# Performance work log

Measured on AMD Instinct MI355X. Metric: run time of the kernel, lower is better.

The kernel has to match this reference:

```python
import jax, jax.numpy as jnp
import numpy as np

N, E = 10000, 320000
IN, HID, HEADS, OUT = 128, 32, 8, 64
NEG_SLOPE = 0.2  # PyG GATv2Conv default negative_slope


def _glorot(k, shape):
    fan = shape[0] + shape[-1]
    return jax.random.normal(k, shape, jnp.float32) * (2.0 / fan) ** 0.5


def setup_inputs() -> dict:
    key = jax.random.key(0)
    ks = jax.random.split(key, 12)
    D2 = HEADS * HID  # 256
    inp = {
        "x": jax.random.normal(ks[0], (N, IN), jnp.float32),
        "edge_index": jax.random.randint(ks[1], (2, E), 0, N, jnp.int32),
        # layer 1: IN -> HID per head, HEADS heads, concat
        "Wl1": _glorot(ks[2], (IN, D2)), "bl1": jnp.zeros((D2,), jnp.float32),
        "Wr1": _glorot(ks[3], (IN, D2)), "br1": jnp.zeros((D2,), jnp.float32),
        "att1": _glorot(ks[4], (HEADS, HID)), "bias1": jnp.zeros((D2,), jnp.float32),
        # layer 2: D2 -> HID per head, HEADS heads, concat
        "Wl2": _glorot(ks[5], (D2, D2)), "bl2": jnp.zeros((D2,), jnp.float32),
        "Wr2": _glorot(ks[6], (D2, D2)), "br2": jnp.zeros((D2,), jnp.float32),
        "att2": _glorot(ks[7], (HEADS, HID)), "bias2": jnp.zeros((D2,), jnp.float32),
        # layer 3: D2 -> OUT, 1 head
        "Wl3": _glorot(ks[8], (D2, OUT)), "bl3": jnp.zeros((OUT,), jnp.float32),
        "Wr3": _glorot(ks[9], (D2, OUT)), "br3": jnp.zeros((OUT,), jnp.float32),
        "att3": _glorot(ks[10], (1, OUT)), "bias3": jnp.zeros((OUT,), jnp.float32),
    }
    return inp


def _segment_softmax(scores, seg, n):
    # softmax over edges grouped by destination node
    m = jax.ops.segment_max(scores, seg, num_segments=n)
    m = jnp.where(jnp.isfinite(m), m, 0.0)  # guard isolated nodes
    ex = jnp.exp(scores - m[seg])
    denom = jax.ops.segment_sum(ex, seg, num_segments=n)
    return ex / (denom[seg] + 1e-16)


def _gatv2_conv(x, src, dst, Wl, bl, Wr, br, att, bias, heads, ch, n):
    gl = (x @ Wl + bl).reshape(n, heads, ch)  # source-side transform [N,H,C]
    gr = (x @ Wr + br).reshape(n, heads, ch)  # target-side transform [N,H,C]
    e = jax.nn.leaky_relu(gl[src] + gr[dst], NEG_SLOPE)  # [E,H,C]
    score = jnp.einsum('ehc,hc->eh', e, att)  # per-edge per-head attention logits
    alpha = _segment_softmax(score, dst, n)  # [E,H]; attention dropout p=0.6 is identity in eval
    out = jax.ops.segment_sum(alpha[:, :, None] * gl[src], dst, num_segments=n)  # [N,H,C]
    return out.reshape(n, heads * ch) + bias


def reference(x, edge_index, Wl1, bl1, Wr1, br1, att1, bias1,
              Wl2, bl2, Wr2, br2, att2, bias2,
              Wl3, bl3, Wr3, br3, att3, bias3):
    src, dst = edge_index[0], edge_index[1]
    n = x.shape[0]
    # F.dropout(p=0.6) layers are identity in eval mode
    h = jax.nn.elu(_gatv2_conv(x, src, dst, Wl1, bl1, Wr1, br1, att1, bias1, HEADS, HID, n))
    h = jax.nn.elu(_gatv2_conv(h, src, dst, Wl2, bl2, Wr2, br2, att2, bias2, HEADS, HID, n))
    h = _gatv2_conv(h, src, dst, Wl3, bl3, Wr3, br3, att3, bias3, 1, OUT, n)
    return jax.nn.sigmoid(h)
```

## Files before the change

### kernel.cpp

```cpp
#include <hip/hip_runtime.h>
#include <math.h>

#define N_NODES 10000
#define N_EDGES 320000
#define D_IN    128
#define D2      256
#define HEADS   8
#define HID     32
#define D_OUT   64

typedef _Float16 h2 __attribute__((ext_vector_type(2)));

__device__ __forceinline__ float fdot2(h2 a, h2 b, float c) {
#if __has_builtin(__builtin_amdgcn_fdot2)
    return __builtin_amdgcn_fdot2(a, b, c, false);
#else
    return fmaf((float)a.x, (float)b.x, fmaf((float)a.y, (float)b.y, c));
#endif
}
__device__ __forceinline__ h2 bch2(unsigned u) { return __builtin_bit_cast(h2, u); }
__device__ __forceinline__ unsigned bcu(h2 v)  { return __builtin_bit_cast(unsigned, v); }
__device__ __forceinline__ unsigned packf(float a, float b) {
    h2 h = {(_Float16)a, (_Float16)b};
    return bcu(h);
}

__global__ void zero_deg(int* __restrict__ deg) {
    const int i = blockIdx.x * 256 + threadIdx.x;
    if (i < N_NODES) deg[i] = 0;
}

__global__ void prep_all(const float* __restrict__ x, unsigned* __restrict__ xh,
                         const float* __restrict__ a1, unsigned* __restrict__ a1h,
                         const float* __restrict__ a2, unsigned* __restrict__ a2h,
                         const float* __restrict__ W1l, const float* __restrict__ W1r,
                         const float* __restrict__ W2l, const float* __restrict__ W2r,
                         const float* __restrict__ W3l, const float* __restrict__ W3r,
                         unsigned* __restrict__ P1l, unsigned* __restrict__ P1r,
                         unsigned* __restrict__ P2l, unsigned* __restrict__ P2r,
                         unsigned* __restrict__ P3l, unsigned* __restrict__ P3r,
                         const int* __restrict__ ei, int* __restrict__ deg) {
    const int b = blockIdx.x, t = threadIdx.x;
    if (b < 2500) {
        const int i = b * 256 + t;
        const float2 f = *reinterpret_cast<const float2*>(&x[2 * i]);
        xh[i] = packf(f.x, f.y);
    } else if (b == 2500) {
        if (t < 128) a1h[t] = packf(a1[2 * t], a1[2 * t + 1]);
    } else if (b == 2501) {
        if (t < 128) a2h[t] = packf(a2[2 * t], a2[2 * t + 1]);
    } else if (b < 2950) {
        const int wb = b - 2502;
        const float* src; unsigned* dst; int M, idx;
        if (wb < 128)      { M = 256; const bool r = wb >= 64;  src = r ? W1r : W1l; dst = r ? P1r : P1l; idx = (wb & 63) * 256 + t; }
        else if (wb < 384) { M = 256; const bool r = wb >= 256; src = r ? W2r : W2l; dst = r ? P2r : P2l; idx = ((wb - 128) & 127) * 256 + t; }
        else               { M = 64;  const bool r = wb >= 416; src = r ? W3r : W3l; dst = r ? P3r : P3l; idx = ((wb - 384) & 31) * 256 + t; }
        const int kp = idx / M, c = idx - kp * M;
        dst[idx] = packf(src[(2 * kp) * M + c], src[(2 * kp + 1) * M + c]);
    } else {
        const int e = (b - 2950) * 256 + t;
        if (e < N_EDGES) atomicAdd(&deg[ei[N_EDGES + e]], 1);
    }
}

template<int K, bool HOUT>
__global__ __launch_bounds__(512) void gemm_dual_fd(
        const unsigned* __restrict__ Ah,
        const unsigned* __restrict__ Wpl, const float* __restrict__ bl,
        const unsigned* __restrict__ Wpr, const float* __restrict__ br,
        void* __restrict__ glv, void* __restrict__ grv,
        int Mtot, int nrows) {
    constexpr int BM = 64, BN = 64, KP = 16;
    constexpr int KPtot = K / 2;
    __shared__ unsigned As2[KP][BM + 1];
    __shared__ unsigned Wls[KP][BN + 4];
    __shared__ unsigned Wrs[KP][BN + 4];

    const int t  = threadIdx.x;
    const int tx = t & 15;
    const int ty = t >> 4;
    const int row0 = blockIdx.x * BM;
    const int col0 = blockIdx.y * BN;

    const int an  = t >> 3;
    const int aq2 = (t & 7) * 2;
    const int sel = t >> 8;
    const int wk  = (t >> 4) & 15;
    const int wc  = (t & 15) * 4;
    const unsigned* Wsrc = sel ? Wpr : Wpl;
    unsigned* wd = sel ? &Wrs[0][0] : &Wls[0][0];

    float aL[2][4], aR[2][4];
    {
        const float4 b4l = *reinterpret_cast<const float4*>(&bl[col0 + tx * 4]);
        const float4 b4r = *reinterpret_cast<const float4*>(&br[col0 + tx * 4]);
        const float bll[4] = {b4l.x, b4l.y, b4l.z, b4l.w};
        const float brr[4] = {b4r.x, b4r.y, b4r.z, b4r.w};
#pragma unroll
        for (int i = 0; i < 2; ++i)
#pragma unroll
            for (int j = 0; j < 4; ++j) { aL[i][j] = bll[j]; aR[i][j] = brr[j]; }
    }

    for (int k0p = 0; k0p < KPtot; k0p += KP) {
        __syncthreads();
        {
            const int row = row0 + an;
            uint2 v = make_uint2(0u, 0u);
            if (row < nrows) v = *reinterpret_cast<const uint2*>(&Ah[(size_t)row * KPtot + k0p + aq2]);
            As2[aq2 + 0][an] = v.x;
            As2[aq2 + 1][an] = v.y;
        }
        {
            const uint4 w = *reinterpret_cast<const uint4*>(&Wsrc[(size_t)(k0p + wk) * Mtot + col0 + wc]);
            *reinterpret_cast<uint4*>(&wd[wk * (BN + 4) + wc]) = w;
        }
        __syncthreads();

#pragma unroll
        for (int kp = 0; kp < KP; ++kp) {
            const h2 a0 = bch2(As2[kp][ty * 2 + 0]);
            const h2 a1 = bch2(As2[kp][ty * 2 + 1]);
            const uint4 lu = *reinterpret_cast<const uint4*>(&Wls[kp][tx * 4]);
            const uint4 ru = *reinterpret_cast<const uint4*>(&Wrs[kp][tx * 4]);
            const h2 l[4] = {bch2(lu.x), bch2(lu.y), bch2(lu.z), bch2(lu.w)};
            const h2 r[4] = {bch2(ru.x), bch2(ru.y), bch2(ru.z), bch2(ru.w)};
#pragma unroll
            for (int j = 0; j < 4; ++j) {
                aL[0][j] = fdot2(a0, l[j], aL[0][j]);
                aL[1][j] = fdot2(a1, l[j], aL[1][j]);
                aR[0][j] = fdot2(a0, r[j], aR[0][j]);
                aR[1][j] = fdot2(a1, r[j], aR[1][j]);
            }
        }
    }

#pragma unroll
    for (int i = 0; i < 2; ++i) {
        const int row = row0 + ty * 2 + i;
        if (row < nrows) {
            if constexpr (HOUT) {
                unsigned* glu = (unsigned*)glv;
                unsigned* gru = (unsigned*)grv;
                const size_t off = (size_t)row * (Mtot / 2) + (col0 + tx * 4) / 2;
                *reinterpret_cast<uint2*>(&glu[off]) =
                    make_uint2(packf(aL[i][0], aL[i][1]), packf(aL[i][2], aL[i][3]));
                *reinterpret_cast<uint2*>(&gru[off]) =
                    make_uint2(packf(aR[i][0], aR[i][1]), packf(aR[i][2], aR[i][3]));
            } else {
                float* glf = (float*)glv;
                float* grf = (float*)grv;
                const size_t off = (size_t)row * Mtot + col0 + tx * 4;
                *reinterpret_cast<float4*>(&glf[off]) = make_float4(aL[i][0], aL[i][1], aL[i][2], aL[i][3]);
                *reinterpret_cast<float4*>(&grf[off]) = make_float4(aR[i][0], aR[i][1], aR[i][2], aR[i][3]);
            }
        }
    }
}

__global__ void scan_rowptr(const int* __restrict__ deg,
                            int* __restrict__ row_ptr, int* __restrict__ cursor) {
    __shared__ int part[1024];
    const int t = threadIdx.x;
    const int base = t * 10;
    int loc[10];
    int s = 0;
#pragma unroll
    for (int i = 0; i < 10; ++i) {
        const int v = (base + i < N_NODES) ? deg[base + i] : 0;
        loc[i] = s; s += v;
    }
    part[t] = s;
    __syncthreads();
    for (int d = 1; d < 1024; d <<= 1) {
        const int v = (t >= d) ? part[t - d] : 0;
        __syncthreads();
        part[t] += v;
        __syncthreads();
    }
    const int off = (t > 0) ? part[t - 1] : 0;
#pragma unroll
    for (int i = 0; i < 10; ++i) {
        const int idx = base + i;
        if (idx < N_NODES) {
            const int r = off + loc[i];
            row_ptr[idx] = r; cursor[idx] = r;
        }
    }
    if (t == 0) row_ptr[N_NODES] = N_EDGES;
}

__global__ void scatter_edges(const int* __restrict__ ei, int* __restrict__ cursor,
                              int* __restrict__ esrc) {
    const int e = blockIdx.x * blockDim.x + threadIdx.x;
    if (e < N_EDGES) {
        const int pos = atomicAdd(&cursor[ei[N_EDGES + e]], 1);
        esrc[pos] = ei[e];
    }
}

__global__ __launch_bounds__(256) void gat_wave_h2(
        const int* __restrict__ row_ptr, const int* __restrict__ esrc,
        const unsigned* __restrict__ gl, const unsigned* __restrict__ gr,
        const unsigned* __restrict__ atth, const float* __restrict__ bias,
        unsigned* __restrict__ hout) {
    constexpr int MU = D2 / 2;
    const int wid  = threadIdx.x >> 6;
    const int lane = threadIdx.x & 63;
    const int half = lane >> 5;
    const int sub  = lane & 31;
    const int n = blockIdx.x * 4 + wid;
    if (n >= N_NODES) return;
    const int u4 = sub * 4;
    const int c0 = sub * 8;

    h2 grn[4], av[4];
    {
        const uint4 u = *reinterpret_cast<const uint4*>(&gr[(size_t)n * MU + u4]);
        grn[0] = bch2(u.x); grn[1] = bch2(u.y); grn[2] = bch2(u.z); grn[3] = bch2(u.w);
        const uint4 a = *reinterpret_cast<const uint4*>(&atth[u4]);
        av[0] = bch2(a.x); av[1] = bch2(a.y); av[2] = bch2(a.z); av[3] = bch2(a.w);
    }
    const h2 hz = {(_Float16)0.f, (_Float16)0.f};
    const h2 hp = {(_Float16)0.2f, (_Float16)0.2f};

    float acc[8] = {0.f, 0.f, 0.f, 0.f, 0.f, 0.f, 0.f, 0.f};
    float denom = 0.0f;

    const int beg = row_ptr[n], end = row_ptr[n + 1];

    for (int base = beg; base < end; base += 64) {
        const int len = min(64, end - base);
        const int npairs = (len + 1) >> 1;
        const int myid = (base + lane < end) ? esrc[base + lane] : 0;

        uint4 cur, nx1;
        {
            const int s0 = __shfl(myid, half);
            cur = *reinterpret_cast<const uint4*>(&gl[(size_t)s0 * MU + u4]);
        }
        if (npairs > 1) {
            const int s1 = __shfl(myid, 2 + half);
            nx1 = *reinterpret_cast<const uint4*>(&gl[(size_t)s1 * MU + u4]);
        } else nx1 = cur;

        for (int i = 0; i < npairs; ++i) {
            uint4 nx2 = cur;
            if (i + 2 < npairs) {
                const int s2 = __shfl(myid, 2 * (i + 2) + half);
                nx2 = *reinterpret_cast<const uint4*>(&gl[(size_t)s2 * MU + u4]);
            }

            const h2 G[4] = {bch2(cur.x), bch2(cur.y), bch2(cur.z), bch2(cur.w)};
            float s = 0.0f;
#pragma unroll
            for (int q = 0; q < 4; ++q) {
                const h2 v = G[q] + grn[q];
                const h2 lr = __builtin_elementwise_min(v, hz) * hp +
                              __builtin_elementwise_max(v, hz);
                s = fdot2(lr, av[q], s);
            }
            s += __shfl_xor(s, 1, 64);
            s += __shfl_xor(s, 2, 64);
            s = ((2 * i + half) < len) ? s : -INFINITY;

            const float e1 = __expf(s);
            denom += e1;
#pragma unroll
            for (int q = 0; q < 4; ++q) {
                acc[2*q]   = fmaf(e1, (float)G[q].x, acc[2*q]);
                acc[2*q+1] = fmaf(e1, (float)G[q].y, acc[2*q+1]);
            }
            cur = nx1; nx1 = nx2;
        }
    }

    denom += __shfl_xor(denom, 32, 64);
#pragma unroll
    for (int v2 = 0; v2 < 8; ++v2) acc[v2] += __shfl_xor(acc[v2], 32, 64);

    if (half == 0) {
        const float inv = 1.0f / (denom + 1e-16f);
        const float4 b0 = *reinterpret_cast<const float4*>(&bias[c0]);
        const float4 b1 = *reinterpret_cast<const float4*>(&bias[c0 + 4]);
        const float bb[8] = {b0.x, b0.y, b0.z, b0.w, b1.x, b1.y, b1.z, b1.w};
        float r[8];
#pragma unroll
        for (int v2 = 0; v2 < 8; ++v2) {
            float val = acc[v2] * inv + bb[v2];
            r[v2] = val > 0.0f ? val : expm1f(val);
        }
        uint4 o;
        o.x = packf(r[0], r[1]); o.y = packf(r[2], r[3]);
        o.z = packf(r[4], r[5]); o.w = packf(r[6], r[7]);
        *reinterpret_cast<uint4*>(&hout[(size_t)n * MU + u4]) = o;
    }
}

__global__ __launch_bounds__(256) void gat_group3(
        const int* __restrict__ row_ptr, const int* __restrict__ esrc,
        const float* __restrict__ gl, const float* __restrict__ gr,
        const float* __restrict__ att, const float* __restrict__ bias,
        float* __restrict__ out) {
    constexpr int M = 64;
    const int wid  = threadIdx.x >> 6;
    const int lane = threadIdx.x & 63;
    const int g    = lane >> 4;
    const int sub  = lane & 15;
    const int n = blockIdx.x * 16 + wid * 4 + g;
    const bool nvalid = (n < N_NODES);
    const int c0 = sub * 4;

    float grn[4], attc[4], acc[4] = {0.f, 0.f, 0.f, 0.f};
    {
        const size_t noff = (size_t)(nvalid ? n : 0) * M + c0;
        const float4 g4 = *reinterpret_cast<const float4*>(&gr[noff]);
        grn[0]=g4.x; grn[1]=g4.y; grn[2]=g4.z; grn[3]=g4.w;
        const float4 a4 = *reinterpret_cast<const float4*>(&att[c0]);
        attc[0]=a4.x; attc[1]=a4.y; attc[2]=a4.z; attc[3]=a4.w;
    }
    float denom = 0.0f;

    const int beg = nvalid ? row_ptr[n] : 0;
    const int deg = nvalid ? (row_ptr[n + 1] - beg) : 0;

    for (int off = 0; __any(off < deg); off += 16) {
        const int myid = (off + sub < deg) ? esrc[beg + off + sub] : 0;

        float4 cur;
        {
            const int src = __shfl(myid, (g << 4));
            cur = *reinterpret_cast<const float4*>(&gl[(size_t)src * M + c0]);
        }
#pragma unroll
        for (int j = 0; j < 16; ++j) {
            float4 nxt = make_float4(0.f, 0.f, 0.f, 0.f);
            if (j + 1 < 16) {
                const int ns = __shfl(myid, (g << 4) + j + 1);
                nxt = *reinterpret_cast<const float4*>(&gl[(size_t)ns * M + c0]);
            }
            const float gg[4] = {cur.x, cur.y, cur.z, cur.w};
            float s = 0.0f;
#pragma unroll
            for (int v = 0; v < 4; ++v) {
                const float val = gg[v] + grn[v];
                const float lr  = fmaxf(val, 0.0f) + 0.2f * fminf(val, 0.0f);
                s = fmaf(lr, attc[v], s);
            }
#pragma unroll
            for (int d = 1; d < 16; d <<= 1) s += __shfl_xor(s, d, 64);
            s = ((off + j) < deg) ? s : -INFINITY;

            const float e1 = __expf(s);
            denom += e1;
#pragma unroll
            for (int v = 0; v < 4; ++v) acc[v] = fmaf(e1, gg[v], acc[v]);
            cur = nxt;
        }
    }

    if (nvalid) {
        const float inv = 1.0f / (denom + 1e-16f);
        float4 r;
        r.x = 1.0f / (1.0f + __expf(-(acc[0] * inv + bias[c0 + 0])));
        r.y = 1.0f / (1.0f + __expf(-(acc[1] * inv + bias[c0 + 1])));
        r.z = 1.0f / (1.0f + __expf(-(acc[2] * inv + bias[c0 + 2])));
        r.w = 1.0f / (1.0f + __expf(-(acc[3] * inv + bias[c0 + 3])));
        *reinterpret_cast<float4*>(&out[(size_t)n * M + c0]) = r;
    }
}

extern "C" void kernel_launch(void* const* d_in, const int* in_sizes, int n_in,
                              void* d_out, int out_size, void* d_ws, size_t ws_size,
                              hipStream_t stream) {
    const float* x    = (const float*)d_in[0];
    const int*   ei   = (const int*)  d_in[1];
    const float* Wl1  = (const float*)d_in[2];
    const float* bl1  = (const float*)d_in[3];
    const float* Wr1  = (const float*)d_in[4];
    const float* br1  = (const float*)d_in[5];
    const float* att1 = (const float*)d_in[6];
    const float* bi1  = (const float*)d_in[7];
    const float* Wl2  = (const float*)d_in[8];
    const float* bl2  = (const float*)d_in[9];
    const float* Wr2  = (const float*)d_in[10];
    const float* br2  = (const float*)d_in[11];
    const float* att2 = (const float*)d_in[12];
    const float* bi2  = (const float*)d_in[13];
    const float* Wl3  = (const float*)d_in[14];
    const float* bl3  = (const float*)d_in[15];
    const float* Wr3  = (const float*)d_in[16];
    const float* br3  = (const float*)d_in[17];
    const float* att3 = (const float*)d_in[18];
    const float* bi3  = (const float*)d_in[19];

    float* out = (float*)d_out;

    unsigned* ws   = (unsigned*)d_ws;
    unsigned* xh   = ws;
    unsigned* gl16 = xh   + (size_t)N_NODES * 64;
    unsigned* gr16 = gl16 + (size_t)N_NODES * 128;
    unsigned* h16  = gr16 + (size_t)N_NODES * 128;
    float*    glf  = (float*)(h16 + (size_t)N_NODES * 128);
    float*    grf  = glf + (size_t)N_NODES * 64;
    unsigned* Wp1l = (unsigned*)(grf + (size_t)N_NODES * 64);
    unsigned* Wp1r = Wp1l + 16384;
    unsigned* Wp2l = Wp1r + 16384;
    unsigned* Wp2r = Wp2l + 32768;
    unsigned* Wp3l = Wp2r + 32768;
    unsigned* Wp3r = Wp3l + 8192;
    unsigned* ath1 = Wp3r + 8192;
    unsigned* ath2 = ath1 + 128;
    int* deg     = (int*)(ath2 + 128);
    int* row_ptr = deg + N_NODES;
    int* cursor  = row_ptr + N_NODES + 1;
    int* esrc    = cursor + N_NODES;

    zero_deg<<<(N_NODES + 255) / 256, 256, 0, stream>>>(deg);
    prep_all<<<2950 + (N_EDGES + 255) / 256, 256, 0, stream>>>(
        x, xh, att1, ath1, att2, ath2,
        Wl1, Wr1, Wl2, Wr2, Wl3, Wr3,
        Wp1l, Wp1r, Wp2l, Wp2r, Wp3l, Wp3r,
        ei, deg);
    scan_rowptr<<<1, 1024, 0, stream>>>(deg, row_ptr, cursor);
    scatter_edges<<<(N_EDGES + 255) / 256, 256, 0, stream>>>(ei, cursor, esrc);

    const int RT64 = (N_NODES + 63) / 64;

    gemm_dual_fd<D_IN, true><<<dim3(RT64, 4), 512, 0, stream>>>(
        xh, Wp1l, bl1, Wp1r, br1, gl16, gr16, D2, N_NODES);
    gat_wave_h2<<<(N_NODES + 3) / 4, 256, 0, stream>>>(
        row_ptr, esrc, gl16, gr16, ath1, bi1, h16);

    gemm_dual_fd<D2, true><<<dim3(RT64, 4), 512, 0, stream>>>(
        h16, Wp2l, bl2, Wp2r, br2, gl16, gr16, D2, N_NODES);
    gat_wave_h2<<<(N_NODES + 3) / 4, 256, 0, stream>>>(
        row_ptr, esrc, gl16, gr16, ath2, bi2, h16);

    gemm_dual_fd<D2, false><<<dim3(RT64, 1), 512, 0, stream>>>(
        h16, Wp3l, bl3, Wp3r, br3, glf, grf, D_OUT, N_NODES);
    gat_group3<<<(N_NODES + 15) / 16, 256, 0, stream>>>(
        row_ptr, esrc, glf, grf, att3, bi3, out);
}
```

Before: 203.3 us.

## Switch dual GEMMs to MFMA with transposed fp16 weights, deepen gather prefetch

Replaces the fdot2-based dual GEMM with a 16x16x32 f16 MFMA kernel. The prep stage now transposes the weights into fp16 column-major tiles through shared memory so they match the MFMA B-operand layout, and the whole A row-tile is staged in LDS once. The edge-gather loops in the layer-1/2 and layer-3 attention kernels also gain a deeper 4-deep register prefetch of source features. This trades scalar dot-product ALU work for matrix cores, at the cost of narrower scalar output stores and more live registers in the gather loops.

```diff
diff --git a/kernel.cpp b/kernel.cpp
--- a/kernel.cpp
+++ b/kernel.cpp
@@ -9,7 +9,9 @@
 #define HID     32
 #define D_OUT   64
 
-typedef _Float16 h2 __attribute__((ext_vector_type(2)));
+typedef _Float16 h2   __attribute__((ext_vector_type(2)));
+typedef _Float16 f16x8 __attribute__((ext_vector_type(8)));
+typedef float    f32x4 __attribute__((ext_vector_type(4)));
 
 __device__ __forceinline__ float fdot2(h2 a, h2 b, float c) {
 #if __has_builtin(__builtin_amdgcn_fdot2)
@@ -19,10 +21,9 @@
 #endif
 }
 __device__ __forceinline__ h2 bch2(unsigned u) { return __builtin_bit_cast(h2, u); }
-__device__ __forceinline__ unsigned bcu(h2 v)  { return __builtin_bit_cast(unsigned, v); }
 __device__ __forceinline__ unsigned packf(float a, float b) {
     h2 h = {(_Float16)a, (_Float16)b};
-    return bcu(h);
+    return __builtin_bit_cast(unsigned, h);
 }
 
 __global__ void zero_deg(int* __restrict__ deg) {
@@ -36,9 +37,9 @@
                          const float* __restrict__ W1l, const float* __restrict__ W1r,
                          const float* __restrict__ W2l, const float* __restrict__ W2r,
                          const float* __restrict__ W3l, const float* __restrict__ W3r,
-                         unsigned* __restrict__ P1l, unsigned* __restrict__ P1r,
-                         unsigned* __restrict__ P2l, unsigned* __restrict__ P2r,
-                         unsigned* __restrict__ P3l, unsigned* __restrict__ P3r,
+                         _Float16* __restrict__ T1l, _Float16* __restrict__ T1r,
+                         _Float16* __restrict__ T2l, _Float16* __restrict__ T2r,
+                         _Float16* __restrict__ T3l, _Float16* __restrict__ T3r,
                          const int* __restrict__ ei, int* __restrict__ deg) {
     const int b = blockIdx.x, t = threadIdx.x;
     if (b < 2500) {
@@ -49,110 +50,100 @@
         if (t < 128) a1h[t] = packf(a1[2 * t], a1[2 * t + 1]);
     } else if (b == 2501) {
         if (t < 128) a2h[t] = packf(a2[2 * t], a2[2 * t + 1]);
-    } else if (b < 2950) {
+    } else if (b < 2558) {
+        __shared__ float tl[64][65];
         const int wb = b - 2502;
-        const float* src; unsigned* dst; int M, idx;
-        if (wb < 128)      { M = 256; const bool r = wb >= 64;  src = r ? W1r : W1l; dst = r ? P1r : P1l; idx = (wb & 63) * 256 + t; }
-        else if (wb < 384) { M = 256; const bool r = wb >= 256; src = r ? W2r : W2l; dst = r ? P2r : P2l; idx = ((wb - 128) & 127) * 256 + t; }
-        else               { M = 64;  const bool r = wb >= 416; src = r ? W3r : W3l; dst = r ? P3r : P3l; idx = ((wb - 384) & 31) * 256 + t; }
-        const int kp = idx / M, c = idx - kp * M;
-        dst[idx] = packf(src[(2 * kp) * M + c], src[(2 * kp + 1) * M + c]);
+        const float* Wsrc; _Float16* Wdst; int K, M, tile;
+        if (wb < 16)      { K = 128; M = 256; const bool r = wb >= 8;  Wsrc = r ? W1r : W1l; Wdst = r ? T1r : T1l; tile = wb & 7; }
+        else if (wb < 48) { K = 256; M = 256; const bool r = wb >= 32; Wsrc = r ? W2r : W2l; Wdst = r ? T2r : T2l; tile = (wb - 16) & 15; }
+        else              { K = 256; M = 64;  const bool r = wb >= 52; Wsrc = r ? W3r : W3l; Wdst = r ? T3r : T3l; tile = (wb - 48) & 3; }
+        const int ktiles = K >> 6;
+        const int k0 = (tile % ktiles) * 64, c0 = (tile / ktiles) * 64;
+        const int rr = t >> 6, cc = t & 63;
+        for (int i = 0; i < 64; i += 4)
+            tl[i + rr][cc] = Wsrc[(size_t)(k0 + i + rr) * M + c0 + cc];
+        __syncthreads();
+        for (int i = 0; i < 64; i += 4)
+            Wdst[(size_t)(c0 + i + rr) * K + k0 + cc] = (_Float16)tl[cc][i + rr];
     } else {
-        const int e = (b - 2950) * 256 + t;
+        const int e = (b - 2558) * 256 + t;
         if (e < N_EDGES) atomicAdd(&deg[ei[N_EDGES + e]], 1);
     }
 }
 
 template<int K, bool HOUT>
-__global__ __launch_bounds__(512) void gemm_dual_fd(
+__global__ __launch_bounds__(256) void gemm_dual_mfma(
         const unsigned* __restrict__ Ah,
-        const unsigned* __restrict__ Wpl, const float* __restrict__ bl,
-        const unsigned* __restrict__ Wpr, const float* __restrict__ br,
+        const _Float16* __restrict__ Wtl, const float* __restrict__ bl,
+        const _Float16* __restrict__ Wtr, const float* __restrict__ br,
         void* __restrict__ glv, void* __restrict__ grv,
         int Mtot, int nrows) {
-    constexpr int BM = 64, BN = 64, KP = 16;
-    constexpr int KPtot = K / 2;
-    __shared__ unsigned As2[KP][BM + 1];
-    __shared__ unsigned Wls[KP][BN + 4];
-    __shared__ unsigned Wrs[KP][BN + 4];
-
-    const int t  = threadIdx.x;
-    const int tx = t & 15;
-    const int ty = t >> 4;
-    const int row0 = blockIdx.x * BM;
-    const int col0 = blockIdx.y * BN;
-
-    const int an  = t >> 3;
-    const int aq2 = (t & 7) * 2;
-    const int sel = t >> 8;
-    const int wk  = (t >> 4) & 15;
-    const int wc  = (t & 15) * 4;
-    const unsigned* Wsrc = sel ? Wpr : Wpl;
-    unsigned* wd = sel ? &Wrs[0][0] : &Wls[0][0];
-
-    float aL[2][4], aR[2][4];
+    constexpr int AS = K + 8;
+    __shared__ __align__(16) _Float16 Asm[64 * AS];
+    __shared__ __align__(16) _Float16 Wsm[2][64 * 40];
+
+    const int t = threadIdx.x;
+    const int wave = t >> 6, lane = t & 63;
+    const int lrow = lane & 15, lgrp = lane >> 4;
+    const int row0 = blockIdx.x * 64, col0 = blockIdx.y * 64;
+
     {
-        const float4 b4l = *reinterpret_cast<const float4*>(&bl[col0 + tx * 4]);
-        const float4 b4r = *reinterpret_cast<const float4*>(&br[col0 + tx * 4]);
-        const float bll[4] = {b4l.x, b4l.y, b4l.z, b4l.w};
-        const float brr[4] = {b4r.x, b4r.y, b4r.z, b4r.w};
-#pragma unroll
-        for (int i = 0; i < 2; ++i)
-#pragma unroll
-            for (int j = 0; j < 4; ++j) { aL[i][j] = bll[j]; aR[i][j] = brr[j]; }
-    }
-
-    for (int k0p = 0; k0p < KPtot; k0p += KP) {
+        constexpr int CPR = K / 8;
+        const int ar = t / CPR, ac = t % CPR;
+        for (int i = 0; i < 64; i += 256 / CPR) {
+            const int row = row0 + i + ar;
+            uint4 v = make_uint4(0u, 0u, 0u, 0u);
+            if (row < nrows) v = *reinterpret_cast<const uint4*>(&Ah[(size_t)row * (K / 2) + ac * 4]);
+            *reinterpret_cast<uint4*>(&Asm[(i + ar) * AS + ac * 8]) = v;
+        }
+    }
+
+    f32x4 accL[4], accR[4];
+#pragma unroll
+    for (int cf = 0; cf < 4; ++cf) { accL[cf] = (f32x4)0.0f; accR[cf] = (f32x4)0.0f; }
+
+    const int wcol = t >> 2, wch = t & 3;
+
+    for (int ks = 0; ks < K / 32; ++ks) {
         __syncthreads();
         {
-            const int row = row0 + an;
-            uint2 v = make_uint2(0u, 0u);
-            if (row < nrows) v = *reinterpret_cast<const uint2*>(&Ah[(size_t)row * KPtot + k0p + aq2]);
-            As2[aq2 + 0][an] = v.x;
-            As2[aq2 + 1][an] = v.y;
-        }
-        {
-            const uint4 w = *reinterpret_cast<const uint4*>(&Wsrc[(size_t)(k0p + wk) * Mtot + col0 + wc]);
-            *reinterpret_cast<uint4*>(&wd[wk * (BN + 4) + wc]) = w;
+            const uint4 vl = *reinterpret_cast<const uint4*>(&Wtl[(size_t)(col0 + wcol) * K + ks * 32 + wch * 8]);
+            const uint4 vr = *reinterpret_cast<const uint4*>(&Wtr[(size_t)(col0 + wcol) * K + ks * 32 + wch * 8]);
+            *reinterpret_cast<uint4*>(&Wsm[0][wcol * 40 + wch * 8]) = vl;
+            *reinterpret_cast<uint4*>(&Wsm[1][wcol * 40 + wch * 8]) = vr;
         }
         __syncthreads();
 
-#pragma unroll
-        for (int kp = 0; kp < KP; ++kp) {
-            const h2 a0 = bch2(As2[kp][ty * 2 + 0]);
-            const h2 a1 = bch2(As2[kp][ty * 2 + 1]);
-            const uint4 lu = *reinterpret_cast<const uint4*>(&Wls[kp][tx * 4]);
-            const uint4 ru = *reinterpret_cast<const uint4*>(&Wrs[kp][tx * 4]);
-            const h2 l[4] = {bch2(lu.x), bch2(lu.y), bch2(lu.z), bch2(lu.w)};
-            const h2 r[4] = {bch2(ru.x), bch2(ru.y), bch2(ru.z), bch2(ru.w)};
-#pragma unroll
-            for (int j = 0; j < 4; ++j) {
-                aL[0][j] = fdot2(a0, l[j], aL[0][j]);
-                aL[1][j] = fdot2(a1, l[j], aL[1][j]);
-                aR[0][j] = fdot2(a0, r[j], aR[0][j]);
-                aR[1][j] = fdot2(a1, r[j], aR[1][j]);
-            }
-        }
-    }
-
-#pragma unroll
-    for (int i = 0; i < 2; ++i) {
-        const int row = row0 + ty * 2 + i;
-        if (row < nrows) {
-            if constexpr (HOUT) {
-                unsigned* glu = (unsigned*)glv;
-                unsigned* gru = (unsigned*)grv;
-                const size_t off = (size_t)row * (Mtot / 2) + (col0 + tx * 4) / 2;
-                *reinterpret_cast<uint2*>(&glu[off]) =
-                    make_uint2(packf(aL[i][0], aL[i][1]), packf(aL[i][2], aL[i][3]));
-                *reinterpret_cast<uint2*>(&gru[off]) =
-                    make_uint2(packf(aR[i][0], aR[i][1]), packf(aR[i][2], aR[i][3]));
-            } else {
-                float* glf = (float*)glv;
-                float* grf = (float*)grv;
-                const size_t off = (size_t)row * Mtot + col0 + tx * 4;
-                *reinterpret_cast<float4*>(&glf[off]) = make_float4(aL[i][0], aL[i][1], aL[i][2], aL[i][3]);
-                *reinterpret_cast<float4*>(&grf[off]) = make_float4(aR[i][0], aR[i][1], aR[i][2], aR[i][3]);
+        const f16x8 a = *reinterpret_cast<const f16x8*>(
+            &Asm[(wave * 16 + lrow) * AS + ks * 32 + lgrp * 8]);
+#pragma unroll
+        for (int cf = 0; cf < 4; ++cf) {
+            const f16x8 b_l = *reinterpret_cast<const f16x8*>(&Wsm[0][(cf * 16 + lrow) * 40 + lgrp * 8]);
+            const f16x8 b_r = *reinterpret_cast<const f16x8*>(&Wsm[1][(cf * 16 + lrow) * 40 + lgrp * 8]);
+            accL[cf] = __builtin_amdgcn_mfma_f32_16x16x32_f16(a, b_l, accL[cf], 0, 0, 0);
+            accR[cf] = __builtin_amdgcn_mfma_f32_16x16x32_f16(a, b_r, accR[cf], 0, 0, 0);
+        }
+    }
+
+#pragma unroll
+    for (int cf = 0; cf < 4; ++cf) {
+        const int col = col0 + cf * 16 + lrow;
+        const float bll = bl[col], brr = br[col];
+#pragma unroll
+        for (int r = 0; r < 4; ++r) {
+            const int row = row0 + wave * 16 + lgrp * 4 + r;
+            if (row < nrows) {
+                if constexpr (HOUT) {
+                    _Float16* glh = (_Float16*)glv;
+                    _Float16* grh = (_Float16*)grv;
+                    glh[(size_t)row * Mtot + col] = (_Float16)(accL[cf][r] + bll);
+                    grh[(size_t)row * Mtot + col] = (_Float16)(accR[cf][r] + brr);
+                } else {
+                    float* glf = (float*)glv;
+                    float* grf = (float*)grv;
+                    glf[(size_t)row * Mtot + col] = accL[cf][r] + bll;
+                    grf[(size_t)row * Mtot + col] = accR[cf][r] + brr;
+                }
             }
         }
     }
@@ -234,24 +225,16 @@
         const int npairs = (len + 1) >> 1;
         const int myid = (base + lane < end) ? esrc[base + lane] : 0;
 
-        uint4 cur, nx1;
-        {
-            const int s0 = __shfl(myid, half);
-            cur = *reinterpret_cast<const uint4*>(&gl[(size_t)s0 * MU + u4]);
-        }
-        if (npairs > 1) {
-            const int s1 = __shfl(myid, 2 + half);
-            nx1 = *reinterpret_cast<const uint4*>(&gl[(size_t)s1 * MU + u4]);
-        } else nx1 = cur;
+#define LOADP(k) (*reinterpret_cast<const uint4*>(&gl[(size_t)__shfl(myid, 2 * (k) + half) * MU + u4]))
+        uint4 g0 = LOADP(0);
+        uint4 g1 = (npairs > 1) ? LOADP(1) : g0;
+        uint4 g2 = (npairs > 2) ? LOADP(2) : g0;
+        uint4 g3 = (npairs > 3) ? LOADP(3) : g0;
 
         for (int i = 0; i < npairs; ++i) {
-            uint4 nx2 = cur;
-            if (i + 2 < npairs) {
-                const int s2 = __shfl(myid, 2 * (i + 2) + half);
-                nx2 = *reinterpret_cast<const uint4*>(&gl[(size_t)s2 * MU + u4]);
-            }
-
-            const h2 G[4] = {bch2(cur.x), bch2(cur.y), bch2(cur.z), bch2(cur.w)};
+            const uint4 nxt = (i + 4 < npairs) ? LOADP(i + 4) : g0;
+
+            const h2 G[4] = {bch2(g0.x), bch2(g0.y), bch2(g0.z), bch2(g0.w)};
             float s = 0.0f;
 #pragma unroll
             for (int q = 0; q < 4; ++q) {
@@ -268,11 +251,12 @@
             denom += e1;
 #pragma unroll
             for (int q = 0; q < 4; ++q) {
-                acc[2*q]   = fmaf(e1, (float)G[q].x, acc[2*q]);
-                acc[2*q+1] = fmaf(e1, (float)G[q].y, acc[2*q+1]);
+                acc[2 * q]     = fmaf(e1, (float)G[q].x, acc[2 * q]);
+                acc[2 * q + 1] = fmaf(e1, (float)G[q].y, acc[2 * q + 1]);
             }
-            cur = nx1; nx1 = nx2;
-        }
+            g0 = g1; g1 = g2; g2 = g3; g3 = nxt;
+        }
+#undef LOADP
     }
 
     denom += __shfl_xor(denom, 32, 64);
@@ -327,19 +311,12 @@
     for (int off = 0; __any(off < deg); off += 16) {
         const int myid = (off + sub < deg) ? esrc[beg + off + sub] : 0;
 
-        float4 cur;
-        {
-            const int src = __shfl(myid, (g << 4));
-            cur = *reinterpret_cast<const float4*>(&gl[(size_t)src * M + c0]);
-        }
+#define GLD(j) (*reinterpret_cast<const float4*>(&gl[(size_t)__shfl(myid, (g << 4) + (j)) * M + c0]))
+        float4 g0 = GLD(0), g1 = GLD(1), g2 = GLD(2), g3 = GLD(3);
 #pragma unroll
         for (int j = 0; j < 16; ++j) {
-            float4 nxt = make_float4(0.f, 0.f, 0.f, 0.f);
-            if (j + 1 < 16) {
-                const int ns = __shfl(myid, (g << 4) + j + 1);
-                nxt = *reinterpret_cast<const float4*>(&gl[(size_t)ns * M + c0]);
-            }
-            const float gg[4] = {cur.x, cur.y, cur.z, cur.w};
+            const float4 nxt = (j + 4 < 16) ? GLD(j + 4) : g0;
+            const float gg[4] = {g0.x, g0.y, g0.z, g0.w};
             float s = 0.0f;
 #pragma unroll
             for (int v = 0; v < 4; ++v) {
@@ -355,8 +332,9 @@
             denom += e1;
 #pragma unroll
             for (int v = 0; v < 4; ++v) acc[v] = fmaf(e1, gg[v], acc[v]);
-            cur = nxt;
-        }
+            g0 = g1; g1 = g2; g2 = g3; g3 = nxt;
+        }
+#undef GLD
     }
 
     if (nvalid) {
@@ -403,13 +381,13 @@
     unsigned* h16  = gr16 + (size_t)N_NODES * 128;
     float*    glf  = (float*)(h16 + (size_t)N_NODES * 128);
     float*    grf  = glf + (size_t)N_NODES * 64;
-    unsigned* Wp1l = (unsigned*)(grf + (size_t)N_NODES * 64);
-    unsigned* Wp1r = Wp1l + 16384;
-    unsigned* Wp2l = Wp1r + 16384;
-    unsigned* Wp2r = Wp2l + 32768;
-    unsigned* Wp3l = Wp2r + 32768;
-    unsigned* Wp3r = Wp3l + 8192;
-    unsigned* ath1 = Wp3r + 8192;
+    _Float16* T1l  = (_Float16*)(grf + (size_t)N_NODES * 64);
+    _Float16* T1r  = T1l + 32768;
+    _Float16* T2l  = T1r + 32768;
+    _Float16* T2r  = T2l + 65536;
+    _Float16* T3l  = T2r + 65536;
+    _Float16* T3r  = T3l + 16384;
+    unsigned* ath1 = (unsigned*)(T3r + 16384);
     unsigned* ath2 = ath1 + 128;
     int* deg     = (int*)(ath2 + 128);
     int* row_ptr = deg + N_NODES;
@@ -417,28 +395,28 @@
     int* esrc    = cursor + N_NODES;
 
     zero_deg<<<(N_NODES + 255) / 256, 256, 0, stream>>>(deg);
-    prep_all<<<2950 + (N_EDGES + 255) / 256, 256, 0, stream>>>(
+    prep_all<<<2558 + (N_EDGES + 255) / 256, 256, 0, stream>>>(
         x, xh, att1, ath1, att2, ath2,
         Wl1, Wr1, Wl2, Wr2, Wl3, Wr3,
-        Wp1l, Wp1r, Wp2l, Wp2r, Wp3l, Wp3r,
+        T1l, T1r, T2l, T2r, T3l, T3r,
         ei, deg);
     scan_rowptr<<<1, 1024, 0, stream>>>(deg, row_ptr, cursor);
     scatter_edges<<<(N_EDGES + 255) / 256, 256, 0, stream>>>(ei, cursor, esrc);
 
     const int RT64 = (N_NODES + 63) / 64;
 
-    gemm_dual_fd<D_IN, true><<<dim3(RT64, 4), 512, 0, stream>>>(
-        xh, Wp1l, bl1, Wp1r, br1, gl16, gr16, D2, N_NODES);
+    gemm_dual_mfma<D_IN, true><<<dim3(RT64, 4), 256, 0, stream>>>(
+        xh, T1l, bl1, T1r, br1, gl16, gr16, D2, N_NODES);
     gat_wave_h2<<<(N_NODES + 3) / 4, 256, 0, stream>>>(
         row_ptr, esrc, gl16, gr16, ath1, bi1, h16);
 
-    gemm_dual_fd<D2, true><<<dim3(RT64, 4), 512, 0, stream>>>(
-        h16, Wp2l, bl2, Wp2r, br2, gl16, gr16, D2, N_NODES);
+    gemm_dual_mfma<D2, true><<<dim3(RT64, 4), 256, 0, stream>>>(
+        h16, T2l, bl2, T2r, br2, gl16, gr16, D2, N_NODES);
     gat_wave_h2<<<(N_NODES + 3) / 4, 256, 0, stream>>>(
         row_ptr, esrc, gl16, gr16, ath2, bi2, h16);
 
-    gemm_dual_fd<D2, false><<<dim3(RT64, 1), 512, 0, stream>>>(
-        h16, Wp3l, bl3, Wp3r, br3, glf, grf, D_OUT, N_NODES);
+    gemm_dual_mfma<D2, false><<<dim3(RT64, 1), 256, 0, stream>>>(
+        h16, T3l, bl3, T3r, br3, glf, grf, D_OUT, N_NODES);
     gat_group3<<<(N_NODES + 15) / 16, 256, 0, stream>>>(
         row_ptr, esrc, glf, grf, att3, bi3, out);
 }
```

Result: faster. 177.8 us (-12.5%).
